# Performance work log

Measured on AMD Instinct MI355X. Metric: run time of the kernel, lower is better.

## Reference

```python
import jax, jax.numpy as jnp
import numpy as np

B, T, HIDDEN = 1, 2048, 2048
N_HEADS, N_KV_HEADS, HEAD_DIM = 32, 8, 64
N_KV_GROUPS = N_HEADS // N_KV_HEADS
MAX_POS = 8192


def _rope_tables(seq_len, head_dim, dtype):
    inv_freq = 1.0 / (10000.0 ** (jnp.arange(0, head_dim, 2, dtype=jnp.float32) / head_dim))
    t = jnp.arange(seq_len, dtype=jnp.float32)
    freqs = jnp.einsum('i,j->ij', t, inv_freq)          # [T, head_dim//2]
    emb = jnp.concatenate([freqs, freqs], axis=-1)      # [T, head_dim]
    cos = jnp.cos(emb)[None, None].astype(dtype)        # [1,1,T,head_dim]
    sin = jnp.sin(emb)[None, None].astype(dtype)
    return cos, sin


def _apply_rotary(x, cos, sin):
    # faithful to original: interleaved rotate-half with cat(freqs,freqs) tables
    x1, x2 = x[..., ::2], x[..., 1::2]
    x_rot = jnp.stack([-x2, x1], axis=-1).reshape(x.shape)
    return x * cos + x_rot * sin


def setup_inputs() -> dict:
    key = jax.random.key(0)
    kx, kq, kk, kv, ko = jax.random.split(key, 5)
    s = 0.02
    return {
        'x':  jax.random.normal(kx, (B, T, HIDDEN), dtype=jnp.float32),
        'Wq': s * jax.random.normal(kq, (N_HEADS * HEAD_DIM, HIDDEN), dtype=jnp.float32),
        'Wk': s * jax.random.normal(kk, (N_KV_HEADS * HEAD_DIM, HIDDEN), dtype=jnp.float32),
        'Wv': s * jax.random.normal(kv, (N_KV_HEADS * HEAD_DIM, HIDDEN), dtype=jnp.float32),
        'Wo': s * jax.random.normal(ko, (HIDDEN, HIDDEN), dtype=jnp.float32),
    }


def reference(x, Wq, Wk, Wv, Wo):
    Bv, Tv, _ = x.shape
    dtype = x.dtype
    # projections (torch Linear: y = x @ W.T), reshape to [B, heads, T, head_dim]
    q = jnp.einsum('bth,oh->bto', x, Wq).reshape(Bv, Tv, N_HEADS, HEAD_DIM).transpose(0, 2, 1, 3)
    k = jnp.einsum('bth,oh->bto', x, Wk).reshape(Bv, Tv, N_KV_HEADS, HEAD_DIM).transpose(0, 2, 1, 3)
    v = jnp.einsum('bth,oh->bto', x, Wv).reshape(Bv, Tv, N_KV_HEADS, HEAD_DIM).transpose(0, 2, 1, 3)
    cos, sin = _rope_tables(Tv, HEAD_DIM, dtype)
    q = _apply_rotary(q, cos, sin)
    k = _apply_rotary(k, cos, sin)
    if N_KV_GROUPS != 1:
        k = jnp.repeat(k, N_KV_GROUPS, axis=1)   # [B, n_heads, T, d]
        v = jnp.repeat(v, N_KV_GROUPS, axis=1)
    scale = 1.0 / jnp.sqrt(jnp.asarray(HEAD_DIM, dtype=dtype))
    scores = jnp.einsum('bhtd,bhsd->bhts', q, k) * scale   # [B,H,T,T]
    causal = jnp.tril(jnp.ones((Tv, Tv), dtype=bool))
    scores = jnp.where(causal[None, None], scores, jnp.asarray(-jnp.inf, dtype=dtype))
    attn = jax.nn.softmax(scores, axis=-1)
    out = jnp.einsum('bhts,bhsd->bhtd', attn, v)
    out = out.transpose(0, 2, 1, 3).reshape(Bv, Tv, HIDDEN)
    return jnp.einsum('bth,oh->bto', out, Wo)
```

## Files before the change

kernel.cpp:

```cpp
#include <hip/hip_runtime.h>
#include <hip/hip_bf16.h>
#include <stdint.h>

#define TT 2048
#define HID 2048
#define NH 32
#define NKV 8
#define HD 64

typedef __attribute__((ext_vector_type(4))) float f32x4;
typedef __attribute__((ext_vector_type(16))) float f32x16;
typedef __attribute__((ext_vector_type(8))) short bf16x8;

__device__ __forceinline__ unsigned short f2bf(float f) {
  unsigned int u = __builtin_bit_cast(unsigned int, f);
  unsigned int r = (u + 0x7FFFu + ((u >> 16) & 1u)) >> 16;
  return (unsigned short)r;
}
__device__ __forceinline__ float bf2f(unsigned short h) {
  unsigned int u = ((unsigned int)h) << 16;
  return __builtin_bit_cast(float, u);
}
__device__ __forceinline__ unsigned int cvtpk(float lo, float hi) {
  unsigned int d;
  asm("v_cvt_pk_bf16_f32 %0, %1, %2" : "=v"(d) : "v"(lo), "v"(hi));
  return d;
}

__device__ __forceinline__ void gld_lds16(const void* g, void* l) {
  __builtin_amdgcn_global_load_lds(
      (const __attribute__((address_space(1))) unsigned int*)g,
      (__attribute__((address_space(3))) unsigned int*)l,
      16, 0, 0);
}

__global__ __launch_bounds__(256)
void k_cvt_all(const float* __restrict__ x, const float* __restrict__ wq,
               const float* __restrict__ wk, const float* __restrict__ wv,
               const float* __restrict__ wo,
               unsigned short* __restrict__ xb, unsigned short* __restrict__ wqb,
               unsigned short* __restrict__ wkb, unsigned short* __restrict__ wvb,
               unsigned short* __restrict__ wob) {
  int i = blockIdx.x * 256 + threadIdx.x;
  const float* src; unsigned short* dst; int off;
  if      (i < 1048576) { src = x;  dst = xb;  off = i; }
  else if (i < 2097152) { src = wq; dst = wqb; off = i - 1048576; }
  else if (i < 2359296) { src = wk; dst = wkb; off = i - 2097152; }
  else if (i < 2621440) { src = wv; dst = wvb; off = i - 2359296; }
  else if (i < 3670016) { src = wo; dst = wob; off = i - 2621440; }
  else return;
  const float4 v = reinterpret_cast<const float4*>(src)[off];
  ushort4 o;
  o.x = f2bf(v.x); o.y = f2bf(v.y); o.z = f2bf(v.z); o.w = f2bf(v.w);
  reinterpret_cast<ushort4*>(dst)[off] = o;
}

__device__ __forceinline__ void stage_tile(const unsigned short* __restrict__ g,
                                           unsigned short* lds, int w, int l, int k0) {
#pragma unroll
  for (int j = 0; j < 2; ++j) {
    const int cbase = w * 128 + j * 64;
    const int c = cbase + l;
    const int row = c >> 2, off = c & 3;
    gld_lds16(g + row * 2048 + k0 + off * 8, lds + cbase * 8);
  }
}

__device__ __forceinline__ void gemm_core(const unsigned short* __restrict__ A,
                                          const unsigned short* __restrict__ B,
                                          unsigned short* As, unsigned short* Bs,
                                          f32x4 (&acc)[4][4], int kiters) {
  const int tid = threadIdx.x;
  const int l = tid & 63, w = tid >> 6;
  const int wm = w >> 1, wn = w & 1;
  const int ll = l & 15, lg = l >> 4;

  stage_tile(A, As, w, l, 0);
  stage_tile(B, Bs, w, l, 0);
  int cur = 0;
  for (int kt = 0; kt < kiters; ++kt) {
    __syncthreads();
    if (kt + 1 < kiters) {
      stage_tile(A, As + (cur ^ 1) * 4096, w, l, (kt + 1) * 32);
      stage_tile(B, Bs + (cur ^ 1) * 4096, w, l, (kt + 1) * 32);
    }
    const unsigned short* a0 = As + cur * 4096;
    const unsigned short* b0 = Bs + cur * 4096;
    bf16x8 af[4], bfr[4];
#pragma unroll
    for (int i = 0; i < 4; ++i) {
      af[i]  = *reinterpret_cast<const bf16x8*>(a0 + (wm * 64 + i * 16 + ll) * 32 + lg * 8);
      bfr[i] = *reinterpret_cast<const bf16x8*>(b0 + (wn * 64 + i * 16 + ll) * 32 + lg * 8);
    }
#pragma unroll
    for (int i = 0; i < 4; ++i)
#pragma unroll
      for (int j = 0; j < 4; ++j)
        acc[i][j] = __builtin_amdgcn_mfma_f32_16x16x32_bf16(af[i], bfr[j], acc[i][j], 0, 0, 0);
    cur ^= 1;
  }
}

__global__ __launch_bounds__(256)
void k_gemm_qkv(const unsigned short* __restrict__ xb,
                const unsigned short* __restrict__ wq,
                const unsigned short* __restrict__ wk,
                const unsigned short* __restrict__ wv,
                unsigned short* __restrict__ Pq,
                unsigned short* __restrict__ Pk,
                unsigned short* __restrict__ Pv) {
  __shared__ __align__(16) unsigned short As[2 * 4096];
  __shared__ __align__(16) unsigned short Bs[2 * 4096];
  const int bid = blockIdx.x;
  const unsigned short *A, *B;
  int m0, n0, seg, ks;
  if (bid < 640) {
    ks = bid & 1;
    int pair = bid >> 1;
    int mt = pair / 20, nt = pair % 20;
    m0 = mt * 128;
    A = xb + (size_t)m0 * 2048 + ks * 1024;
    if (nt < 16) { seg = 0; n0 = nt * 128; B = wq + (size_t)n0 * 2048 + ks * 1024; }
    else         { seg = 1; n0 = (nt - 16) * 128; B = wk + (size_t)n0 * 2048 + ks * 1024; }
  } else {
    int vb = bid - 640;
    ks = vb & 1;
    int pair = vb >> 1;
    int mt = pair / 16, nt = pair % 16;
    seg = 2; m0 = mt * 128; n0 = nt * 128;
    A = wv + (size_t)m0 * 2048 + ks * 1024;
    B = xb + (size_t)n0 * 2048 + ks * 1024;
  }
  f32x4 acc[4][4] = {};
  gemm_core(A, B, As, Bs, acc, 32);

  const int l = threadIdx.x & 63, w = threadIdx.x >> 6;
  const int wm = w >> 1, wn = w & 1;
#pragma unroll
  for (int i = 0; i < 4; ++i)
#pragma unroll
    for (int j = 0; j < 4; ++j)
#pragma unroll
      for (int r = 0; r < 4; ++r) {
        int row = m0 + wm * 64 + i * 16 + ((l >> 4) << 2) + r;
        int col = n0 + wn * 64 + j * 16 + (l & 15);
        unsigned short v = f2bf(acc[i][j][r]);
        if (seg == 0)      Pq[(size_t)ks * 4194304 + (size_t)row * 2048 + col] = v;
        else if (seg == 1) Pk[(size_t)ks * 1048576 + (size_t)row * 512 + col] = v;
        else               Pv[(size_t)ks * 1048576 + (size_t)row * 2048 + col] = v;
      }
}

__global__ __launch_bounds__(256)
void k_gemm_out(const unsigned short* __restrict__ Ob,
                const unsigned short* __restrict__ wo,
                float* __restrict__ out,
                unsigned short* __restrict__ P1,
                unsigned short* __restrict__ P2) {
  __shared__ __align__(16) unsigned short As[2 * 4096];
  __shared__ __align__(16) unsigned short Bs[2 * 4096];
  const int bid = blockIdx.x;
  const int ks = bid >> 8;
  const int rem = bid & 255;
  const int m0 = (rem >> 4) * 128, n0 = (rem & 15) * 128;
  const int k0 = (ks == 0) ? 0 : 704 + (ks - 1) * 672;
  const int kiters = (ks == 0) ? 22 : 21;
  f32x4 acc[4][4] = {};
  gemm_core(Ob + (size_t)m0 * 2048 + k0,
            wo + (size_t)n0 * 2048 + k0, As, Bs, acc, kiters);

  const int l = threadIdx.x & 63, w = threadIdx.x >> 6;
  const int wm = w >> 1, wn = w & 1;
#pragma unroll
  for (int i = 0; i < 4; ++i)
#pragma unroll
    for (int j = 0; j < 4; ++j)
#pragma unroll
      for (int r = 0; r < 4; ++r) {
        int row = m0 + wm * 64 + i * 16 + ((l >> 4) << 2) + r;
        int col = n0 + wn * 64 + j * 16 + (l & 15);
        if (ks == 0)      out[(size_t)row * HID + col] = acc[i][j][r];
        else if (ks == 1) P1[(size_t)row * HID + col] = f2bf(acc[i][j][r]);
        else              P2[(size_t)row * HID + col] = f2bf(acc[i][j][r]);
      }
}

__global__ __launch_bounds__(256)
void k_reduce_out(float* __restrict__ out,
                  const unsigned short* __restrict__ P1,
                  const unsigned short* __restrict__ P2) {
  const int i = blockIdx.x * 256 + threadIdx.x;
  float4 a = reinterpret_cast<const float4*>(out)[i];
  const ushort4 b = reinterpret_cast<const ushort4*>(P1)[i];
  const ushort4 c = reinterpret_cast<const ushort4*>(P2)[i];
  a.x += bf2f(b.x) + bf2f(c.x);
  a.y += bf2f(b.y) + bf2f(c.y);
  a.z += bf2f(b.z) + bf2f(c.z);
  a.w += bf2f(b.w) + bf2f(c.w);
  reinterpret_cast<float4*>(out)[i] = a;
}

__global__ __launch_bounds__(256)
void k_rope_tab(float2* __restrict__ tab) {
  const int i = blockIdx.x * 256 + threadIdx.x;
  const int t = i >> 6, k = i & 63;
  const float cexp = -13.287712379549449f / 32.0f;
  const float fr = exp2f((float)(k & 31) * cexp);
  const float a = (float)t * fr;
  tab[i] = make_float2(__cosf(a), __sinf(a));
}

__global__ __launch_bounds__(256)
void k_rope_apply(const unsigned short* __restrict__ Pk,
                  const unsigned short* __restrict__ Pv,
                  const unsigned short* __restrict__ Pq,
                  const float2* __restrict__ tab,
                  unsigned short* __restrict__ Kb,
                  unsigned short* __restrict__ VT,
                  unsigned short* __restrict__ Qb) {
  int p = blockIdx.x * 256 + threadIdx.x;
  if (p < 524288) {
    const int t = p >> 8;
    const int col2 = (p & 255) * 2;
    const int kh = col2 >> 6, d = col2 & 63;
    const unsigned int u0 = *reinterpret_cast<const unsigned int*>(Pk + (size_t)t * 512 + col2);
    const unsigned int u1 = *reinterpret_cast<const unsigned int*>(Pk + 1048576 + (size_t)t * 512 + col2);
    float x0 = bf2f((unsigned short)(u0 & 0xFFFFu)) + bf2f((unsigned short)(u1 & 0xFFFFu));
    float x1 = bf2f((unsigned short)(u0 >> 16)) + bf2f((unsigned short)(u1 >> 16));
    const float4 cs = *reinterpret_cast<const float4*>(tab + t * 64 + d);
    float o0 = x0 * cs.x - x1 * cs.y;
    float o1 = x1 * cs.z + x0 * cs.w;
    unsigned int pw = (unsigned int)f2bf(o0) | ((unsigned int)f2bf(o1) << 16);
    *reinterpret_cast<unsigned int*>(Kb + ((size_t)kh * 2048 + t) * 64 + d) = pw;
  } else if (p < 1048576) {
    const int i2 = (p - 524288) * 2;
    const unsigned int u0 = *reinterpret_cast<const unsigned int*>(Pv + i2);
    const unsigned int u1 = *reinterpret_cast<const unsigned int*>(Pv + 1048576 + i2);
    float x0 = bf2f((unsigned short)(u0 & 0xFFFFu)) + bf2f((unsigned short)(u1 & 0xFFFFu));
    float x1 = bf2f((unsigned short)(u0 >> 16)) + bf2f((unsigned short)(u1 >> 16));
    unsigned int pw = (unsigned int)f2bf(x0) | ((unsigned int)f2bf(x1) << 16);
    *reinterpret_cast<unsigned int*>(VT + i2) = pw;
  } else {
    const int pq = p - 1048576;
    const int t = pq >> 10;
    const int col2 = (pq & 1023) * 2;
    const int h = col2 >> 6, d = col2 & 63;
    const unsigned int u0 = *reinterpret_cast<const unsigned int*>(Pq + (size_t)t * 2048 + col2);
    const unsigned int u1 = *reinterpret_cast<const unsigned int*>(Pq + 4194304 + (size_t)t * 2048 + col2);
    float x0 = bf2f((unsigned short)(u0 & 0xFFFFu)) + bf2f((unsigned short)(u1 & 0xFFFFu));
    float x1 = bf2f((unsigned short)(u0 >> 16)) + bf2f((unsigned short)(u1 >> 16));
    const float scale = 0.125f * 1.4426950408889634f;
    const float4 cs = *reinterpret_cast<const float4*>(tab + t * 64 + d);
    float o0 = (x0 * cs.x - x1 * cs.y) * scale;
    float o1 = (x1 * cs.z + x0 * cs.w) * scale;
    unsigned int pw = (unsigned int)f2bf(o0) | ((unsigned int)f2bf(o1) << 16);
    *reinterpret_cast<unsigned int*>(Qb + ((size_t)h * 2048 + t) * 64 + d) = pw;
  }
}

__device__ __forceinline__ void attn_stage(const unsigned short* __restrict__ Kg,
                                           const unsigned short* __restrict__ Vg,
                                           unsigned short* Ks, unsigned short* Vs,
                                           int kv0, int w, int l) {
#pragma unroll
  for (int j = 0; j < 4; ++j) {
    const int cb = j * 128 + w * 64;
    const int c = cb + l;
    const int row = c >> 3;
    const int src8 = ((c & 7) ^ (row & 7)) * 8;
    gld_lds16(Kg + (size_t)(kv0 + row) * 64 + src8, Ks + cb * 8);
    gld_lds16(Vg + (size_t)row * TT + kv0 + src8, Vs + cb * 8);
  }
}

__global__ __launch_bounds__(128, 2)
void k_attn(const unsigned short* __restrict__ Qb,
            const unsigned short* __restrict__ Kb,
            const unsigned short* __restrict__ VT,
            unsigned short* __restrict__ Ob) {
  __shared__ __align__(16) unsigned short Ks[2][64 * 64];
  __shared__ __align__(16) unsigned short Vs[2][64 * 64];
  const int b = blockIdx.x;
  const int h = b & 31;
  const int qi = b >> 5;
  const int q0 = qi & 7, kq = qi >> 3;
  const int qt = (kq == 0) ? 2 * q0 : (kq == 1) ? 31 - 2 * q0
               : (kq == 2) ? 2 * q0 + 1 : 30 - 2 * q0;
  const int kh = h >> 2;
  const int tid = threadIdx.x;
  const int l = tid & 63, w = tid >> 6;
  const int q = l & 31, hi = l >> 5;
  const int qrow = qt * 64 + w * 32 + q;

  const unsigned short* Qh = Qb + (size_t)h * TT * 64;
  const unsigned short* Kh = Kb + (size_t)kh * TT * 64;
  const unsigned short* Vh = VT + (size_t)kh * 64 * TT;

  bf16x8 qf[4];
#pragma unroll
  for (int s = 0; s < 4; ++s)
    qf[s] = *reinterpret_cast<const bf16x8*>(Qh + (size_t)qrow * 64 + s * 16 + hi * 8);

  f32x16 ot0, ot1;
#pragma unroll
  for (int r = 0; r < 16; ++r) { ot0[r] = 0.f; ot1[r] = 0.f; }
  float lsum = 0.f;
  const int nkt = qt + 1;

  attn_stage(Kh, Vh, Ks[0], Vs[0], 0, w, l);
  int cur = 0;
  for (int kt = 0; kt < nkt; ++kt) {
    __syncthreads();
    if (kt + 1 < nkt)
      attn_stage(Kh, Vh, Ks[cur ^ 1], Vs[cur ^ 1], (kt + 1) * 64, w, l);

    const char* Kc = reinterpret_cast<const char*>(Ks[cur]);
    const char* Vc = reinterpret_cast<const char*>(Vs[cur]);

    f32x16 s0, s1;
#pragma unroll
    for (int r = 0; r < 16; ++r) { s0[r] = 0.f; s1[r] = 0.f; }
    __builtin_amdgcn_s_setprio(1);
#pragma unroll
    for (int s = 0; s < 4; ++s) {
      const int chunk = 2 * s + hi;
      const bf16x8 kf0 = *reinterpret_cast<const bf16x8*>(
          Kc + q * 128 + ((chunk ^ (q & 7)) * 16));
      const bf16x8 kf1 = *reinterpret_cast<const bf16x8*>(
          Kc + (32 + q) * 128 + ((chunk ^ (q & 7)) * 16));
      s0 = __builtin_amdgcn_mfma_f32_32x32x16_bf16(kf0, qf[s], s0, 0, 0, 0);
      s1 = __builtin_amdgcn_mfma_f32_32x32x16_bf16(kf1, qf[s], s1, 0, 0, 0);
    }
    __builtin_amdgcn_s_setprio(0);
    if (kt == qt) {
#pragma unroll
      for (int r = 0; r < 16; ++r) {
        const int kvr = kt * 64 + (r & 3) + 8 * (r >> 2) + 4 * hi;
        if (kvr > qrow) s0[r] = -3e38f;
        if (kvr + 32 > qrow) s1[r] = -3e38f;
      }
    }
#pragma unroll
    for (int r = 0; r < 16; ++r) {
      s0[r] = __builtin_amdgcn_exp2f(s0[r] - 16.f);
      s1[r] = __builtin_amdgcn_exp2f(s1[r] - 16.f);
    }
    float t16[16];
#pragma unroll
    for (int r = 0; r < 16; ++r) t16[r] = s0[r] + s1[r];
#pragma unroll
    for (int r = 0; r < 8; ++r) t16[r] += t16[r + 8];
#pragma unroll
    for (int r = 0; r < 4; ++r) t16[r] += t16[r + 4];
    lsum += (t16[0] + t16[1]) + (t16[2] + t16[3]);

#pragma unroll
    for (int s = 0; s < 4; ++s) {
      const int base = (s & 1) * 8;
      const f32x16& sg = (s < 2) ? s0 : s1;
      const unsigned int c0 = cvtpk(sg[base + 0], sg[base + 1]);
      const unsigned int c1 = cvtpk(sg[base + 2], sg[base + 3]);
      const unsigned int c2 = cvtpk(sg[base + 4], sg[base + 5]);
      const unsigned int c3 = cvtpk(sg[base + 6], sg[base + 7]);
      const unsigned int slo = hi ? c0 : c2, shi_ = hi ? c1 : c3;
      const unsigned int rlo = (unsigned int)__shfl_xor((int)slo, 32);
      const unsigned int rhi = (unsigned int)__shfl_xor((int)shi_, 32);
      union { unsigned int u[4]; bf16x8 v; } P;
      P.u[0] = hi ? rlo : c0;
      P.u[1] = hi ? rhi : c1;
      P.u[2] = hi ? c2 : rlo;
      P.u[3] = hi ? c3 : rhi;
      const int chunk = 2 * s + hi;
      const bf16x8 vf0 = *reinterpret_cast<const bf16x8*>(
          Vc + q * 128 + ((chunk ^ (q & 7)) * 16));
      const bf16x8 vf1 = *reinterpret_cast<const bf16x8*>(
          Vc + (32 + q) * 128 + ((chunk ^ (q & 7)) * 16));
      __builtin_amdgcn_s_setprio(1);
      ot0 = __builtin_amdgcn_mfma_f32_32x32x16_bf16(vf0, P.v, ot0, 0, 0, 0);
      ot1 = __builtin_amdgcn_mfma_f32_32x32x16_bf16(vf1, P.v, ot1, 0, 0, 0);
      __builtin_amdgcn_s_setprio(0);
    }
    cur ^= 1;
  }

  lsum += __shfl_xor(lsum, 32);
  __syncthreads();
  float* Of = reinterpret_cast<float*>(&Ks[0][0]) + w * (64 * 33);
  const float inv = 1.0f / lsum;
#pragma unroll
  for (int r = 0; r < 16; ++r) {
    const int d = (r & 3) + 8 * (r >> 2) + 4 * hi;
    Of[d * 33 + q] = ot0[r] * inv;
    Of[(d + 32) * 33 + q] = ot1[r] * inv;
  }
  __syncthreads();
#pragma unroll
  for (int i = 0; i < 4; ++i) {
    const int a = 4 * hi + i;
    float v[8];
#pragma unroll
    for (int k2 = 0; k2 < 8; ++k2) v[k2] = Of[(a * 8 + k2) * 33 + q];
    union { unsigned int u[4]; uint4 vec; } O4;
    O4.u[0] = cvtpk(v[0], v[1]);
    O4.u[1] = cvtpk(v[2], v[3]);
    O4.u[2] = cvtpk(v[4], v[5]);
    O4.u[3] = cvtpk(v[6], v[7]);
    *reinterpret_cast<uint4*>(Ob + (size_t)qrow * HID + h * 64 + a * 8) = O4.vec;
  }
}

extern "C" void kernel_launch(void* const* d_in, const int* in_sizes, int n_in,
                              void* d_out, int out_size, void* d_ws, size_t ws_size,
                              hipStream_t stream) {
  const float* x  = (const float*)d_in[0];
  const float* Wq = (const float*)d_in[1];
  const float* Wk = (const float*)d_in[2];
  const float* Wv = (const float*)d_in[3];
  const float* Wo = (const float*)d_in[4];
  float* out = (float*)d_out;
  char* ws = (char*)d_ws;

  unsigned short* xb  = (unsigned short*)(ws);
  unsigned short* wqb = (unsigned short*)(ws + (8u  << 20));
  unsigned short* wkb = (unsigned short*)(ws + (16u << 20));
  unsigned short* wvb = (unsigned short*)(ws + (18u << 20));
  unsigned short* wob = (unsigned short*)(ws + (20u << 20));
  unsigned short* Kb  = (unsigned short*)(ws + (36u << 20));
  unsigned short* VT  = (unsigned short*)(ws + (38u << 20));
  unsigned short* Ob  = xb;
  unsigned short* Qb  = (unsigned short*)(ws + (8u << 20));
  float2* tab = (float2*)(ws + (16u << 20));
  unsigned short* Pq = (unsigned short*)d_out;
  unsigned short* Pk = (unsigned short*)(ws + (28u << 20));
  unsigned short* Pv = (unsigned short*)(ws + (32u << 20));
  unsigned short* P1 = (unsigned short*)(ws + (28u << 20));
  unsigned short* P2 = (unsigned short*)(ws + (8u  << 20));

  k_cvt_all<<<14336, 256, 0, stream>>>(x, Wq, Wk, Wv, Wo, xb, wqb, wkb, wvb, wob);
  k_gemm_qkv<<<768, 256, 0, stream>>>(xb, wqb, wkb, wvb, Pq, Pk, Pv);
  k_rope_tab<<<512, 256, 0, stream>>>(tab);
  k_rope_apply<<<12288, 256, 0, stream>>>(Pk, Pv, Pq, tab, Kb, VT, Qb);
  k_attn<<<1024, 128, 0, stream>>>(Qb, Kb, VT, Ob);
  k_gemm_out<<<768, 256, 0, stream>>>(Ob, wob, out, P1, P2);
  k_reduce_out<<<4096, 256, 0, stream>>>(out, P1, P2);
}
```

Measured before the change: 155.4 us.

## Merge two query tiles per attention block to share K/V staging

Each attention block now has four waves covering two adjacent 64-row query tiles (128 rows) instead of two waves covering one tile. The staged K/V tiles in LDS are shared across both query tiles, which halves global K/V loads per query row and halves the grid size, with a new reversed-pair ordering for load balance. Waves on the lower query tile sit idle on the final KV tile, and the shared memory region grows to fit four waves' output staging.

```diff
diff --git a/kernel.cpp b/kernel.cpp
--- a/kernel.cpp
+++ b/kernel.cpp
@@ -258,13 +258,13 @@
   }
 }
 
-__device__ __forceinline__ void attn_stage(const unsigned short* __restrict__ Kg,
-                                           const unsigned short* __restrict__ Vg,
-                                           unsigned short* Ks, unsigned short* Vs,
-                                           int kv0, int w, int l) {
-#pragma unroll
-  for (int j = 0; j < 4; ++j) {
-    const int cb = j * 128 + w * 64;
+__device__ __forceinline__ void attn_stage4(const unsigned short* __restrict__ Kg,
+                                            const unsigned short* __restrict__ Vg,
+                                            unsigned short* Ks, unsigned short* Vs,
+                                            int kv0, int w, int l) {
+#pragma unroll
+  for (int j = 0; j < 2; ++j) {
+    const int cb = j * 256 + w * 64;
     const int c = cb + l;
     const int row = c >> 3;
     const int src8 = ((c & 7) ^ (row & 7)) * 8;
@@ -273,24 +273,25 @@
   }
 }
 
-__global__ __launch_bounds__(128, 2)
+__global__ __launch_bounds__(256, 2)
 void k_attn(const unsigned short* __restrict__ Qb,
             const unsigned short* __restrict__ Kb,
             const unsigned short* __restrict__ VT,
             unsigned short* __restrict__ Ob) {
-  __shared__ __align__(16) unsigned short Ks[2][64 * 64];
-  __shared__ __align__(16) unsigned short Vs[2][64 * 64];
+  __shared__ __align__(16) unsigned short S[17408];
+  unsigned short* KsB = S;
+  unsigned short* VsB = S + 8192;
   const int b = blockIdx.x;
   const int h = b & 31;
-  const int qi = b >> 5;
-  const int q0 = qi & 7, kq = qi >> 3;
-  const int qt = (kq == 0) ? 2 * q0 : (kq == 1) ? 31 - 2 * q0
-               : (kq == 2) ? 2 * q0 + 1 : 30 - 2 * q0;
+  const int i = b >> 5;
+  const int p = (i < 8) ? (15 - i) : (i - 8);
   const int kh = h >> 2;
   const int tid = threadIdx.x;
   const int l = tid & 63, w = tid >> 6;
   const int q = l & 31, hi = l >> 5;
-  const int qrow = qt * 64 + w * 32 + q;
+  const int qtw = 2 * p + (w >> 1);
+  const int qrow = qtw * 64 + (w & 1) * 32 + q;
+  const int nkt = 2 * p + 2;
 
   const unsigned short* Qh = Qb + (size_t)h * TT * 64;
   const unsigned short* Kh = Kb + (size_t)kh * TT * 64;
@@ -305,87 +306,89 @@
 #pragma unroll
   for (int r = 0; r < 16; ++r) { ot0[r] = 0.f; ot1[r] = 0.f; }
   float lsum = 0.f;
-  const int nkt = qt + 1;
-
-  attn_stage(Kh, Vh, Ks[0], Vs[0], 0, w, l);
+
+  attn_stage4(Kh, Vh, KsB, VsB, 0, w, l);
   int cur = 0;
   for (int kt = 0; kt < nkt; ++kt) {
     __syncthreads();
     if (kt + 1 < nkt)
-      attn_stage(Kh, Vh, Ks[cur ^ 1], Vs[cur ^ 1], (kt + 1) * 64, w, l);
-
-    const char* Kc = reinterpret_cast<const char*>(Ks[cur]);
-    const char* Vc = reinterpret_cast<const char*>(Vs[cur]);
-
-    f32x16 s0, s1;
-#pragma unroll
-    for (int r = 0; r < 16; ++r) { s0[r] = 0.f; s1[r] = 0.f; }
-    __builtin_amdgcn_s_setprio(1);
-#pragma unroll
-    for (int s = 0; s < 4; ++s) {
-      const int chunk = 2 * s + hi;
-      const bf16x8 kf0 = *reinterpret_cast<const bf16x8*>(
-          Kc + q * 128 + ((chunk ^ (q & 7)) * 16));
-      const bf16x8 kf1 = *reinterpret_cast<const bf16x8*>(
-          Kc + (32 + q) * 128 + ((chunk ^ (q & 7)) * 16));
-      s0 = __builtin_amdgcn_mfma_f32_32x32x16_bf16(kf0, qf[s], s0, 0, 0, 0);
-      s1 = __builtin_amdgcn_mfma_f32_32x32x16_bf16(kf1, qf[s], s1, 0, 0, 0);
-    }
-    __builtin_amdgcn_s_setprio(0);
-    if (kt == qt) {
+      attn_stage4(Kh, Vh, KsB + (cur ^ 1) * 4096, VsB + (cur ^ 1) * 4096,
+                  (kt + 1) * 64, w, l);
+
+    if (kt <= qtw) {
+      const char* Kc = reinterpret_cast<const char*>(KsB + cur * 4096);
+      const char* Vc = reinterpret_cast<const char*>(VsB + cur * 4096);
+
+      f32x16 s0, s1;
+#pragma unroll
+      for (int r = 0; r < 16; ++r) { s0[r] = 0.f; s1[r] = 0.f; }
+      __builtin_amdgcn_s_setprio(1);
+#pragma unroll
+      for (int s = 0; s < 4; ++s) {
+        const int chunk = 2 * s + hi;
+        const bf16x8 kf0 = *reinterpret_cast<const bf16x8*>(
+            Kc + q * 128 + ((chunk ^ (q & 7)) * 16));
+        const bf16x8 kf1 = *reinterpret_cast<const bf16x8*>(
+            Kc + (32 + q) * 128 + ((chunk ^ (q & 7)) * 16));
+        s0 = __builtin_amdgcn_mfma_f32_32x32x16_bf16(kf0, qf[s], s0, 0, 0, 0);
+        s1 = __builtin_amdgcn_mfma_f32_32x32x16_bf16(kf1, qf[s], s1, 0, 0, 0);
+      }
+      __builtin_amdgcn_s_setprio(0);
+      if (kt == qtw) {
+#pragma unroll
+        for (int r = 0; r < 16; ++r) {
+          const int kvr = kt * 64 + (r & 3) + 8 * (r >> 2) + 4 * hi;
+          if (kvr > qrow) s0[r] = -3e38f;
+          if (kvr + 32 > qrow) s1[r] = -3e38f;
+        }
+      }
 #pragma unroll
       for (int r = 0; r < 16; ++r) {
-        const int kvr = kt * 64 + (r & 3) + 8 * (r >> 2) + 4 * hi;
-        if (kvr > qrow) s0[r] = -3e38f;
-        if (kvr + 32 > qrow) s1[r] = -3e38f;
-      }
-    }
-#pragma unroll
-    for (int r = 0; r < 16; ++r) {
-      s0[r] = __builtin_amdgcn_exp2f(s0[r] - 16.f);
-      s1[r] = __builtin_amdgcn_exp2f(s1[r] - 16.f);
-    }
-    float t16[16];
-#pragma unroll
-    for (int r = 0; r < 16; ++r) t16[r] = s0[r] + s1[r];
-#pragma unroll
-    for (int r = 0; r < 8; ++r) t16[r] += t16[r + 8];
-#pragma unroll
-    for (int r = 0; r < 4; ++r) t16[r] += t16[r + 4];
-    lsum += (t16[0] + t16[1]) + (t16[2] + t16[3]);
-
-#pragma unroll
-    for (int s = 0; s < 4; ++s) {
-      const int base = (s & 1) * 8;
-      const f32x16& sg = (s < 2) ? s0 : s1;
-      const unsigned int c0 = cvtpk(sg[base + 0], sg[base + 1]);
-      const unsigned int c1 = cvtpk(sg[base + 2], sg[base + 3]);
-      const unsigned int c2 = cvtpk(sg[base + 4], sg[base + 5]);
-      const unsigned int c3 = cvtpk(sg[base + 6], sg[base + 7]);
-      const unsigned int slo = hi ? c0 : c2, shi_ = hi ? c1 : c3;
-      const unsigned int rlo = (unsigned int)__shfl_xor((int)slo, 32);
-      const unsigned int rhi = (unsigned int)__shfl_xor((int)shi_, 32);
-      union { unsigned int u[4]; bf16x8 v; } P;
-      P.u[0] = hi ? rlo : c0;
-      P.u[1] = hi ? rhi : c1;
-      P.u[2] = hi ? c2 : rlo;
-      P.u[3] = hi ? c3 : rhi;
-      const int chunk = 2 * s + hi;
-      const bf16x8 vf0 = *reinterpret_cast<const bf16x8*>(
-          Vc + q * 128 + ((chunk ^ (q & 7)) * 16));
-      const bf16x8 vf1 = *reinterpret_cast<const bf16x8*>(
-          Vc + (32 + q) * 128 + ((chunk ^ (q & 7)) * 16));
-      __builtin_amdgcn_s_setprio(1);
-      ot0 = __builtin_amdgcn_mfma_f32_32x32x16_bf16(vf0, P.v, ot0, 0, 0, 0);
-      ot1 = __builtin_amdgcn_mfma_f32_32x32x16_bf16(vf1, P.v, ot1, 0, 0, 0);
-      __builtin_amdgcn_s_setprio(0);
+        s0[r] = __builtin_amdgcn_exp2f(s0[r] - 16.f);
+        s1[r] = __builtin_amdgcn_exp2f(s1[r] - 16.f);
+      }
+      float t16[16];
+#pragma unroll
+      for (int r = 0; r < 16; ++r) t16[r] = s0[r] + s1[r];
+#pragma unroll
+      for (int r = 0; r < 8; ++r) t16[r] += t16[r + 8];
+#pragma unroll
+      for (int r = 0; r < 4; ++r) t16[r] += t16[r + 4];
+      lsum += (t16[0] + t16[1]) + (t16[2] + t16[3]);
+
+#pragma unroll
+      for (int s = 0; s < 4; ++s) {
+        const int base = (s & 1) * 8;
+        const f32x16& sg = (s < 2) ? s0 : s1;
+        const unsigned int c0 = cvtpk(sg[base + 0], sg[base + 1]);
+        const unsigned int c1 = cvtpk(sg[base + 2], sg[base + 3]);
+        const unsigned int c2 = cvtpk(sg[base + 4], sg[base + 5]);
+        const unsigned int c3 = cvtpk(sg[base + 6], sg[base + 7]);
+        const unsigned int slo = hi ? c0 : c2, shi_ = hi ? c1 : c3;
+        const unsigned int rlo = (unsigned int)__shfl_xor((int)slo, 32);
+        const unsigned int rhi = (unsigned int)__shfl_xor((int)shi_, 32);
+        union { unsigned int u[4]; bf16x8 v; } P;
+        P.u[0] = hi ? rlo : c0;
+        P.u[1] = hi ? rhi : c1;
+        P.u[2] = hi ? c2 : rlo;
+        P.u[3] = hi ? c3 : rhi;
+        const int chunk = 2 * s + hi;
+        const bf16x8 vf0 = *reinterpret_cast<const bf16x8*>(
+            Vc + q * 128 + ((chunk ^ (q & 7)) * 16));
+        const bf16x8 vf1 = *reinterpret_cast<const bf16x8*>(
+            Vc + (32 + q) * 128 + ((chunk ^ (q & 7)) * 16));
+        __builtin_amdgcn_s_setprio(1);
+        ot0 = __builtin_amdgcn_mfma_f32_32x32x16_bf16(vf0, P.v, ot0, 0, 0, 0);
+        ot1 = __builtin_amdgcn_mfma_f32_32x32x16_bf16(vf1, P.v, ot1, 0, 0, 0);
+        __builtin_amdgcn_s_setprio(0);
+      }
     }
     cur ^= 1;
   }
 
   lsum += __shfl_xor(lsum, 32);
   __syncthreads();
-  float* Of = reinterpret_cast<float*>(&Ks[0][0]) + w * (64 * 33);
+  float* Of = reinterpret_cast<float*>(S) + w * (64 * 33);
   const float inv = 1.0f / lsum;
 #pragma unroll
   for (int r = 0; r < 16; ++r) {
@@ -395,8 +398,8 @@
   }
   __syncthreads();
 #pragma unroll
-  for (int i = 0; i < 4; ++i) {
-    const int a = 4 * hi + i;
+  for (int i2 = 0; i2 < 4; ++i2) {
+    const int a = 4 * hi + i2;
     float v[8];
 #pragma unroll
     for (int k2 = 0; k2 < 8; ++k2) v[k2] = Of[(a * 8 + k2) * 33 + q];
@@ -440,7 +443,7 @@
   k_gemm_qkv<<<768, 256, 0, stream>>>(xb, wqb, wkb, wvb, Pq, Pk, Pv);
   k_rope_tab<<<512, 256, 0, stream>>>(tab);
   k_rope_apply<<<12288, 256, 0, stream>>>(Pk, Pv, Pq, tab, Kb, VT, Qb);
-  k_attn<<<1024, 128, 0, stream>>>(Qb, Kb, VT, Ob);
+  k_attn<<<512, 256, 0, stream>>>(Qb, Kb, VT, Ob);
   k_gemm_out<<<768, 256, 0, stream>>>(Ob, wob, out, P1, P2);
   k_reduce_out<<<4096, 256, 0, stream>>>(out, P1, P2);
 }
```

Measured after the change: 149.1 us. -4.1%, faster.
